# Optimization experiments

Hardware: AMD Instinct MI355X
Metric: run time of the kernel (lower is better)

The kernel has to match this reference:

```python
import jax, jax.numpy as jnp
import numpy as np
from jax import lax

D3 = 48      # manifold_dim * 3
M = 512      # mem_slots
H = 256      # slot_dim
K = 32       # topk
IN = 1024    # input_dim
ODE_HID = 128
ODE_STEPS = 2
ODE_DT = 0.5
TEMP = 1.0   # temperature buffer
LN_EPS = 1e-5


def _ln(x, g, b):
    m = jnp.mean(x, axis=-1, keepdims=True)
    v = jnp.mean(jnp.square(x - m), axis=-1, keepdims=True)
    return (x - m) * lax.rsqrt(v + LN_EPS) * g + b


def setup_inputs() -> dict:
    key = jax.random.key(0)
    ks = jax.random.split(key, 12)
    s_in = 1.0 / np.sqrt(IN)
    s_h = 1.0 / np.sqrt(H)
    s_d3 = 1.0 / np.sqrt(D3)
    s_ode = 1.0 / np.sqrt(ODE_HID)
    return {
        "x": jax.random.normal(ks[0], (16, 2048, IN), jnp.float32),
        "w1": jax.random.uniform(ks[1], (IN, D3), jnp.float32, -s_in, s_in),
        "b1": jnp.zeros((D3,), jnp.float32),
        "g1": jnp.ones((D3,), jnp.float32),
        "be1": jnp.zeros((D3,), jnp.float32),
        "wa": jax.random.uniform(ks[2], (D3, ODE_HID), jnp.float32, -s_d3, s_d3),
        "ba": jnp.zeros((ODE_HID,), jnp.float32),
        "wb": jax.random.uniform(ks[3], (ODE_HID, D3), jnp.float32, -s_ode, s_ode),
        "bb": jnp.zeros((D3,), jnp.float32),
        "mem": jax.random.normal(ks[4], (M, H), jnp.float32),
        "pos": jax.random.normal(ks[5], (M, 16, 3), jnp.float32),
        "curv": jax.random.normal(ks[6], (M, 16), jnp.float32),
        "alpha": jnp.float32(0.1),
        "wo": jax.random.uniform(ks[7], (H, IN), jnp.float32, -s_h, s_h),
        "bo": jnp.zeros((IN,), jnp.float32),
        "go": jnp.ones((IN,), jnp.float32),
        "beo": jnp.zeros((IN,), jnp.float32),
    }


def reference(x, w1, b1, g1, be1, wa, ba, wb, bb, mem, pos, curv, alpha, wo, bo, go, beo):
    # manifold projection: Linear -> LayerNorm -> GELU, viewed as (B,S,D,3)
    h = jax.nn.gelu(_ln(x @ w1 + b1, g1, be1), approximate=False)  # (B,S,48)
    # ODE evolution (2 fixed steps over the flattened manifold coords)
    for _ in range(ODE_STEPS):
        dx = jnp.tanh(h @ wa + ba) @ wb + bb
        h = h + ODE_DT * dx
    # attend: query side is detached in the original
    q = lax.stop_gradient(h)                       # (B,S,48)
    mem_pos = pos.reshape(M, -1)                   # (512,48)
    # squared pairwise L2: ||q||^2 - 2 q.m + ||m||^2
    dist = (jnp.sum(q * q, axis=-1, keepdims=True)
            - 2.0 * jnp.einsum('bsd,md->bsm', q, mem_pos)
            + jnp.sum(mem_pos * mem_pos, axis=-1))
    dist = jnp.maximum(dist, 0.0) / max(TEMP, 1e-6)
    curv_w = jnp.exp(-alpha * jnp.linalg.norm(curv, axis=-1))  # (512,)
    dist = dist * curv_w[None, None, :]
    # topk smallest distances
    neg_top, itop = lax.top_k(-dist, K)            # (B,S,K)
    w = jax.nn.softmax(neg_top, axis=-1)           # softmax(-dtop)
    slots = mem[itop]                              # (B,S,K,256) gather
    attended = jnp.einsum('bsk,bskh->bsh', w, slots)
    # output projection: Linear -> LayerNorm -> GELU
    return jax.nn.gelu(_ln(attended @ wo + bo, go, beo), approximate=False)
```

## Files before the change

### kernel.cpp

```cpp
#include <hip/hip_runtime.h>
#include <stdint.h>

typedef unsigned short u16;
typedef __attribute__((ext_vector_type(4))) short short4v;
typedef __attribute__((ext_vector_type(8))) short short8v;
typedef __attribute__((ext_vector_type(4))) float f32x4;
typedef __attribute__((address_space(1))) void gv;
typedef __attribute__((address_space(3))) void lv;

#define NTOK 32768

__device__ __forceinline__ float bf2f(u16 u){ return __uint_as_float(((uint32_t)u)<<16); }
__device__ __forceinline__ u16 f2bf(float f){
  uint32_t u = __float_as_uint(f);
  u += 0x7FFFu + ((u>>16)&1u);
  return (u16)(u>>16);
}
__device__ __forceinline__ void hilo(float v, u16& h, u16& l){
  h = f2bf(v);
  l = f2bf(v - bf2f(h));
}
__device__ __forceinline__ void tsplit(float v, u16& h, u16& l){
  uint32_t b = __float_as_uint(v);
  h = (u16)(b >> 16);
  float lf = v - __uint_as_float(b & 0xFFFF0000u);
  l = (u16)(__float_as_uint(lf) >> 16);
}
__device__ __forceinline__ void tpack8(float4 a, float4 b, short8v& hi, short8v& lo){
  float v[8] = {a.x,a.y,a.z,a.w,b.x,b.y,b.z,b.w};
  #pragma unroll
  for (int i=0;i<8;++i){ u16 h,l; tsplit(v[i],h,l); hi[i]=(short)h; lo[i]=(short)l; }
}
__device__ __forceinline__ float gelu_f(float v){ return 0.5f*v*(1.0f + erff(v*0.70710678118654752440f)); }
__device__ __forceinline__ float gelu_t(float x){
  float u = 0.7978845608028654f*(x + 0.044715f*x*x*x);
  float t = 1.0f - 2.0f/(__expf(2.0f*u) + 1.0f);
  return 0.5f*x*(1.0f + t);
}
__device__ __forceinline__ float tanh_f(float x){ return 1.0f - 2.0f/(__expf(2.0f*x)+1.0f); }

__global__ __launch_bounds__(256) void k_prep(
    const float* __restrict__ w1, const float* __restrict__ wa, const float* __restrict__ wb,
    const float* __restrict__ pos, const float* __restrict__ curv,
    const float* __restrict__ mem, const float* __restrict__ wo,
    const float* __restrict__ alpha,
    u16* __restrict__ w1s, u16* __restrict__ wah, u16* __restrict__ wbh,
    float2* __restrict__ mnw,
    u16* __restrict__ memb, u16* __restrict__ woB, u16* __restrict__ posB)
{
  int i = blockIdx.x*256 + threadIdx.x;
  if (i < 49152){ int n = i>>10, k = i&1023; u16 h,l; hilo(w1[k*48+n], h, l);
                  w1s[i] = h; w1s[49152+i] = l; return; }
  i -= 49152;
  if (i < 8192){ int u = i>>6, d = i&63; float v = (d<48) ? wa[d*128+u] : 0.f;
                 u16 h,l; hilo(v,h,l); wah[i] = h; wah[8192+i] = l; return; }
  i -= 8192;
  if (i < 6144){ int n = i>>7, u = i&127; u16 h,l; hilo(wb[u*48+n], h, l);
                 wbh[i] = h; wbh[6144+i] = l; return; }
  i -= 6144;
  if (i < 512){
    float s = 0.f;
    #pragma unroll
    for (int d=0; d<48; ++d){ float v = pos[i*48+d]; s += v*v; }
    float c2 = 0.f;
    #pragma unroll
    for (int d=0; d<16; ++d){ float v = curv[i*16+d]; c2 += v*v; }
    mnw[i] = make_float2(s, expf(-alpha[0]*sqrtf(c2)));
    return;
  }
  i -= 512;
  if (i < 131072){ memb[i] = f2bf(mem[i]); return; }
  i -= 131072;
  if (i < 262144){
    int e = i & 7, ln = (i>>3)&63, n = (i>>9)&15, cpq = (i>>13)&3, kt = i>>15;
    int col = cpq*256 + n*16 + (ln & 15);
    int k   = kt*32 + (ln >> 4)*8 + e;
    woB[i] = f2bf(wo[k*1024 + col]);
    return;
  }
  i -= 262144;
  if (i < 32768){
    int e = i & 7, ln = (i>>3)&63, n = (i>>9)&31, ks = i>>14;
    int slot = n*16 + (ln&15);
    int d = ks*32 + (ln>>4)*8 + e;
    float v = (d < 48) ? pos[slot*48 + d] : 0.f;
    u16 h,l; hilo(v,h,l);
    posB[i] = h; posB[32768+i] = l;
  }
}

__global__ __launch_bounds__(256, 2) void k_proj(
    const float* __restrict__ x, const u16* __restrict__ w1s,
    const float* __restrict__ b1, const float* __restrict__ g1, const float* __restrict__ be1,
    float* __restrict__ hout)
{
  extern __shared__ char dynp[];
  float* xsl = (float*)dynp;
  u16*   bsl = (u16*)(dynp + 49152);

  const int tid = threadIdx.x;
  const int lane = tid & 63, w = tid >> 6;
  const int l15 = lane & 15, l4 = lane >> 4;
  const int bm = blockIdx.x;
  const int arow = w*16 + l15;

  f32x4 acc[3];
  #pragma unroll
  for (int n=0; n<3; ++n) acc[n] = (f32x4){0.f,0.f,0.f,0.f};

  auto stage_x = [&](float* dst, int kt){
    #pragma unroll
    for (int j=0; j<4; ++j){
      int idx = (j*4 + w)*64 + lane;
      int row = idx >> 4, q = idx & 15;
      int chunk = q >> 1, half = q & 1;
      const float* src = x + (size_t)(bm*64 + row)*1024 + kt*64 + ((chunk ^ (row & 7))*8 + half*4);
      __builtin_amdgcn_global_load_lds((gv*)src, (lv*)(dst + (j*4 + w)*256), 16, 0, 0);
    }
  };
  auto stage_b = [&](u16* dst, int kt){
    #pragma unroll
    for (int j=0; j<3; ++j){
      int idx = (j*4 + w)*64 + lane;
      int hl = (idx >= 384) ? 1 : 0;
      int rr = idx - hl*384;
      int row = rr >> 3, ch = rr & 7;
      const u16* src = w1s + hl*49152 + (size_t)row*1024 + kt*64 + ((ch ^ (row & 7))*8);
      __builtin_amdgcn_global_load_lds((gv*)src, (lv*)(dst + (j*4 + w)*512), 16, 0, 0);
    }
  };
  auto mfma_from = [&](const float* xb, const u16* bb){
    #pragma unroll
    for (int kq=0; kq<2; ++kq){
      int chunk = kq*4 + l4;
      int phys = chunk ^ (arow & 7);
      const float* xa = xb + arow*64 + phys*8;
      float4 a0 = *(const float4*)xa;
      float4 a1 = *(const float4*)(xa + 4);
      short8v ah, al; tpack8(a0, a1, ah, al);
      #pragma unroll
      for (int n=0; n<3; ++n){
        int brow = n*16 + l15;
        int bcx = chunk ^ (brow & 7);
        short8v bh = *(const short8v*)(bb + brow*64 + bcx*8);
        short8v bl = *(const short8v*)(bb + 3072 + brow*64 + bcx*8);
        acc[n] = __builtin_amdgcn_mfma_f32_16x16x32_bf16(ah, bh, acc[n], 0, 0, 0);
        acc[n] = __builtin_amdgcn_mfma_f32_16x16x32_bf16(ah, bl, acc[n], 0, 0, 0);
        acc[n] = __builtin_amdgcn_mfma_f32_16x16x32_bf16(al, bh, acc[n], 0, 0, 0);
      }
    }
  };

  float* x0 = xsl;         float* x1 = xsl + 4096;  float* x2 = xsl + 8192;
  u16*   b0 = bsl;         u16*   b1b = bsl + 6144;

  stage_b(b0, 0);
  stage_x(x0, 0);
  stage_x(x1, 1);

  float* xc = x0; float* xn = x1; float* xn2 = x2;
  u16* bc = b0;  u16* bn = b1b;

  for (int kt = 0; kt < 15; ++kt){
    asm volatile("s_waitcnt vmcnt(4)" ::: "memory");
    __builtin_amdgcn_s_barrier();
    __builtin_amdgcn_sched_barrier(0);
    mfma_from(xc, bc);
    stage_b(bn, kt + 1);
    if (kt < 14) stage_x(xn2, kt + 2);
    { float* t = xc; xc = xn; xn = xn2; xn2 = t; }
    { u16* t = bc; bc = bn; bn = t; }
  }
  asm volatile("s_waitcnt vmcnt(0)" ::: "memory");
  __builtin_amdgcn_s_barrier();
  __builtin_amdgcn_sched_barrier(0);
  mfma_from(xc, bc);

  float b1r[3], g1r[3], e1r[3];
  #pragma unroll
  for (int n=0; n<3; ++n){ int c = n*16 + l15; b1r[n] = b1[c]; g1r[n] = g1[c]; e1r[n] = be1[c]; }
  #pragma unroll
  for (int r=0; r<4; ++r){
    float a0 = acc[0][r] + b1r[0];
    float a1 = acc[1][r] + b1r[1];
    float a2 = acc[2][r] + b1r[2];
    float s1 = a0+a1+a2;
    float s2 = a0*a0 + a1*a1 + a2*a2;
    #pragma unroll
    for (int m=1; m<16; m<<=1){ s1 += __shfl_xor(s1, m); s2 += __shfl_xor(s2, m); }
    float mean = s1 * (1.f/48.f);
    float var  = s2 * (1.f/48.f) - mean*mean;
    float rs = rsqrtf(var + 1e-5f);
    int row = bm*64 + w*16 + l4*4 + r;
    float* hb = hout + (size_t)row*48;
    hb[l15]      = gelu_f((a0-mean)*rs*g1r[0] + e1r[0]);
    hb[16+l15]   = gelu_f((a1-mean)*rs*g1r[1] + e1r[1]);
    hb[32+l15]   = gelu_f((a2-mean)*rs*g1r[2] + e1r[2]);
  }
}

__global__ __launch_bounds__(256) void k_ode(
    const float* __restrict__ hin,
    const u16* __restrict__ wah, const u16* __restrict__ wbh,
    const float* __restrict__ ba, const float* __restrict__ bb,
    float* __restrict__ hout, float* __restrict__ q2b)
{
  extern __shared__ u16 sm[];
  u16* t_hi = sm;
  u16* t_lo = sm + 16384;
  u16* h_hi = sm + 32768;
  u16* h_lo = sm + 40960;
  float* hscr = (float*)sm;

  const int tid = threadIdx.x;
  const int lane = tid & 63, w = tid >> 6;
  const int l15 = lane & 15, l4 = lane >> 4;
  const int bm = blockIdx.x;

  float4 hv4[6];
  #pragma unroll
  for (int it=0; it<6; ++it){
    int q = it*256 + tid;
    int row = q/12, c4 = q - row*12;
    hv4[it] = *(const float4*)(hin + (size_t)(bm*128 + row)*48 + c4*4);
  }
  #pragma unroll
  for (int it=0; it<6; ++it){
    int q = it*256 + tid;
    int row = q/12, c4 = q - row*12;
    *(float4*)&hscr[row*48 + c4*4] = hv4[it];
    float4 v = hv4[it];
    u16 h0,l0,h1,l1,h2,l2,h3,l3;
    tsplit(v.x,h0,l0); tsplit(v.y,h1,l1); tsplit(v.z,h2,l2); tsplit(v.w,h3,l3);
    int off = row*64 + ((c4>>1) ^ (row & 7))*8 + (c4 & 1)*4;
    short4v hv = {(short)h0,(short)h1,(short)h2,(short)h3};
    short4v lv = {(short)l0,(short)l1,(short)l2,(short)l3};
    *(short4v*)&h_hi[off] = hv;
    *(short4v*)&h_lo[off] = lv;
  }
  {
    int row = tid >> 1, ch = 6 + (tid & 1);
    int off = row*64 + (ch ^ (row & 7))*8;
    uint4 z = {0u,0u,0u,0u};
    *(uint4*)&h_hi[off] = z;
    *(uint4*)&h_lo[off] = z;
  }
  __syncthreads();

  float hreg[2][3][4];
  #pragma unroll
  for (int m=0; m<2; ++m)
    #pragma unroll
    for (int n=0; n<3; ++n)
      #pragma unroll
      for (int r=0; r<4; ++r)
        hreg[m][n][r] = hscr[(w*32 + m*16 + l4*4 + r)*48 + n*16 + l15];
  __syncthreads();

  float ba_r[8], bb_r[3];
  #pragma unroll
  for (int n=0; n<8; ++n) ba_r[n] = ba[n*16 + l15];
  #pragma unroll
  for (int n=0; n<3; ++n) bb_r[n] = bb[n*16 + l15];

  for (int s=0; s<2; ++s){
    f32x4 at[2][8];
    #pragma unroll
    for (int m=0; m<2; ++m)
      #pragma unroll
      for (int n=0; n<8; ++n) at[m][n] = (f32x4){0.f,0.f,0.f,0.f};
    #pragma unroll
    for (int kq=0; kq<2; ++kq){
      short8v ah[2], al[2];
      #pragma unroll
      for (int m=0; m<2; ++m){
        int arow = w*32 + m*16 + l15;
        int ac = (kq*4 + l4) ^ (arow & 7);
        ah[m] = *(const short8v*)&h_hi[arow*64 + ac*8];
        al[m] = *(const short8v*)&h_lo[arow*64 + ac*8];
      }
      #pragma unroll
      for (int n=0; n<8; ++n){
        const u16* bp = wah + (n*16 + l15)*64 + kq*32 + l4*8;
        short8v bh = *(const short8v*)bp;
        short8v bl = *(const short8v*)(bp + 8192);
        #pragma unroll
        for (int m=0; m<2; ++m){
          at[m][n] = __builtin_amdgcn_mfma_f32_16x16x32_bf16(ah[m], bh, at[m][n], 0, 0, 0);
          at[m][n] = __builtin_amdgcn_mfma_f32_16x16x32_bf16(ah[m], bl, at[m][n], 0, 0, 0);
          at[m][n] = __builtin_amdgcn_mfma_f32_16x16x32_bf16(al[m], bh, at[m][n], 0, 0, 0);
        }
      }
    }
    #pragma unroll
    for (int m=0; m<2; ++m)
      #pragma unroll
      for (int n=0; n<8; ++n)
        #pragma unroll
        for (int r=0; r<4; ++r){
          float tv = tanh_f(at[m][n][r] + ba_r[n]);
          u16 th, tl; tsplit(tv, th, tl);
          int row = w*32 + m*16 + l4*4 + r;
          int col = n*16 + l15;
          int c = col >> 3;
          int phys = (c & 8) | ((c & 7) ^ (row & 7));
          int off = row*128 + phys*8 + (col & 7);
          t_hi[off] = th; t_lo[off] = tl;
        }
    __syncthreads();
    f32x4 ad[2][3];
    #pragma unroll
    for (int m=0; m<2; ++m)
      #pragma unroll
      for (int n=0; n<3; ++n) ad[m][n] = (f32x4){0.f,0.f,0.f,0.f};
    #pragma unroll
    for (int kq=0; kq<4; ++kq){
      short8v ah[2], al[2];
      #pragma unroll
      for (int m=0; m<2; ++m){
        int arow = w*32 + m*16 + l15;
        int c = kq*4 + l4;
        int phys = (c & 8) | ((c & 7) ^ (arow & 7));
        ah[m] = *(const short8v*)&t_hi[arow*128 + phys*8];
        al[m] = *(const short8v*)&t_lo[arow*128 + phys*8];
      }
      #pragma unroll
      for (int n=0; n<3; ++n){
        const u16* bp = wbh + (n*16 + l15)*128 + kq*32 + l4*8;
        short8v bh = *(const short8v*)bp;
        short8v bl = *(const short8v*)(bp + 6144);
        #pragma unroll
        for (int m=0; m<2; ++m){
          ad[m][n] = __builtin_amdgcn_mfma_f32_16x16x32_bf16(ah[m], bh, ad[m][n], 0, 0, 0);
          ad[m][n] = __builtin_amdgcn_mfma_f32_16x16x32_bf16(ah[m], bl, ad[m][n], 0, 0, 0);
          ad[m][n] = __builtin_amdgcn_mfma_f32_16x16x32_bf16(al[m], bh, ad[m][n], 0, 0, 0);
        }
      }
    }
    #pragma unroll
    for (int m=0; m<2; ++m)
      #pragma unroll
      for (int n=0; n<3; ++n)
        #pragma unroll
        for (int r=0; r<4; ++r)
          hreg[m][n][r] += 0.5f*(ad[m][n][r] + bb_r[n]);
    if (s == 0){
      #pragma unroll
      for (int m=0; m<2; ++m)
        #pragma unroll
        for (int n=0; n<3; ++n)
          #pragma unroll
          for (int r=0; r<4; ++r){
            u16 hh, hl2; tsplit(hreg[m][n][r], hh, hl2);
            int row = w*32 + m*16 + l4*4 + r;
            int col = n*16 + l15;
            int off = row*64 + ((col>>3) ^ (row & 7))*8 + (col & 7);
            h_hi[off] = hh; h_lo[off] = hl2;
          }
      __syncthreads();
    }
  }
  #pragma unroll
  for (int m=0; m<2; ++m){
    #pragma unroll
    for (int r=0; r<4; ++r){
      size_t row = (size_t)(bm*128 + w*32 + m*16 + l4*4 + r);
      #pragma unroll
      for (int n=0; n<3; ++n)
        hout[row*64 + n*16 + l15] = hreg[m][n][r];
      hout[row*64 + 48 + l15] = 0.f;
      float s2 = hreg[m][0][r]*hreg[m][0][r] + hreg[m][1][r]*hreg[m][1][r] + hreg[m][2][r]*hreg[m][2][r];
      #pragma unroll
      for (int msk=1; msk<16; msk<<=1) s2 += __shfl_xor(s2, msk);
      if (l15 == 0) q2b[row] = s2;
    }
  }
}

__global__ __launch_bounds__(256, 4) void k_sel(
    const float* __restrict__ h, const float* __restrict__ q2b,
    const u16* __restrict__ posB, const float2* __restrict__ mnw,
    uint32_t* __restrict__ glist)
{
  __shared__ __align__(16) uint32_t tokKeys[2*4*528];

  const int tid = threadIdx.x;
  const int lane = tid & 63, w = tid >> 6;
  const int g = w >> 1, s = w & 1;
  const int l15 = lane & 15, l4 = lane >> 4;
  const int bm = blockIdx.x;

  const float* hrow = h + (size_t)(bm*32 + g*16 + l15)*64;
  float4 x0 = *(const float4*)(hrow + l4*8);
  float4 x1 = *(const float4*)(hrow + l4*8 + 4);
  float4 x2 = *(const float4*)(hrow + 32 + l4*8);
  float4 x3 = *(const float4*)(hrow + 32 + l4*8 + 4);
  short8v ah0, al0, ah1, al1;
  tpack8(x0, x1, ah0, al0);
  tpack8(x2, x3, ah1, al1);

  float4 q2v = *(const float4*)(q2b + bm*32 + g*16 + l4*4);
  float q2a[4] = {q2v.x, q2v.y, q2v.z, q2v.w};

  uint32_t kk[16][4];
  #pragma unroll
  for (int n=0; n<16; ++n){
    const u16* pb = posB + (size_t)(s*16 + n)*512 + lane*8;
    short8v bh0 = *(const short8v*)(pb);
    short8v bl0 = *(const short8v*)(pb + 32768);
    short8v bh1 = *(const short8v*)(pb + 16384);
    short8v bl1 = *(const short8v*)(pb + 49152);
    f32x4 acc = (f32x4){0.f,0.f,0.f,0.f};
    acc = __builtin_amdgcn_mfma_f32_16x16x32_bf16(ah0, bh0, acc, 0, 0, 0);
    acc = __builtin_amdgcn_mfma_f32_16x16x32_bf16(ah0, bl0, acc, 0, 0, 0);
    acc = __builtin_amdgcn_mfma_f32_16x16x32_bf16(al0, bh0, acc, 0, 0, 0);
    acc = __builtin_amdgcn_mfma_f32_16x16x32_bf16(ah1, bh1, acc, 0, 0, 0);
    acc = __builtin_amdgcn_mfma_f32_16x16x32_bf16(ah1, bl1, acc, 0, 0, 0);
    acc = __builtin_amdgcn_mfma_f32_16x16x32_bf16(al1, bh1, acc, 0, 0, 0);
    const int slot = s*256 + n*16 + l15;
    float2 mw = mnw[slot];
    #pragma unroll
    for (int r=0; r<4; ++r){
      float dd = fmaxf(q2a[r] + mw.x - 2.f*acc[r], 0.f) * mw.y;
      kk[n][r] = (__float_as_uint(dd) & 0xFFFFFE00u) | (uint32_t)slot;
    }
  }

  const int gbase = g*2112;
  const unsigned long long ltmask = (lane == 63) ? 0x7FFFFFFFFFFFFFFFull : ((1ull << lane) - 1ull);
  #pragma unroll
  for (int r=0; r<4; ++r){
    __syncthreads();
    #pragma unroll
    for (int n=0; n<16; ++n)
      tokKeys[gbase + l4*528 + s*256 + n*16 + l15] = kk[n][r];
    __syncthreads();
    uint32_t key8[2][8];
    #pragma unroll
    for (int j=0; j<2; ++j){
      *(uint4*)&key8[j][0] = *(const uint4*)&tokKeys[gbase + (s*2+j)*528 + lane*8];
      *(uint4*)&key8[j][4] = *(const uint4*)&tokKeys[gbase + (s*2+j)*528 + lane*8 + 4];
    }
    uint32_t p[2] = {0u,0u};
    for (int b=30; b>=0; --b){
      #pragma unroll
      for (int j=0; j<2; ++j){
        uint32_t c = p[j] | (1u<<b);
        int cnt = 0;
        #pragma unroll
        for (int i=0; i<8; ++i) cnt += (int)__popcll(__ballot(key8[j][i] < c));
        if (cnt <= 31) p[j] = c;
      }
    }
    #pragma unroll
    for (int j=0; j<2; ++j){
      size_t tok = (size_t)bm*32 + g*16 + (s*2+j)*4 + r;
      int base = 0;
      #pragma unroll
      for (int i=0; i<8; ++i){
        unsigned long long bal = __ballot(key8[j][i] <= p[j]);
        if (key8[j][i] <= p[j]){
          int idx = base + (int)__popcll(bal & ltmask);
          glist[tok*32 + idx] = key8[j][i];
        }
        base += (int)__popcll(bal);
      }
    }
  }
}

__global__ __launch_bounds__(256) void k_attend(
    const uint32_t* __restrict__ glist, const u16* __restrict__ memb,
    u16* __restrict__ att)
{
  const int lane = threadIdx.x & 63, w = threadIdx.x >> 6;
  const size_t tok = (size_t)blockIdx.x*4 + w;
  uint32_t lk[32];
  const uint4* lp = (const uint4*)(glist + tok*32);
  #pragma unroll
  for (int q=0; q<8; ++q) *(uint4*)&lk[q*4] = lp[q];
  uint32_t km = lk[0];
  #pragma unroll
  for (int i=1; i<32; ++i) km = min(km, lk[i]);
  const float dminf = __uint_as_float(km & 0xFFFFFE00u);

  float den = 0.f, a0=0.f, a1=0.f, a2=0.f, a3=0.f;
  #pragma unroll
  for (int i=0; i<32; ++i){
    float dk = __uint_as_float(lk[i] & 0xFFFFFE00u);
    int slot = (int)(lk[i] & 511u);
    float wg = __expf(dminf - dk);
    den += wg;
    uint2 mv = ((const uint2*)(memb + (size_t)slot*256))[lane];
    a0 += wg*bf2f((u16)(mv.x & 0xFFFFu));
    a1 += wg*bf2f((u16)(mv.x >> 16));
    a2 += wg*bf2f((u16)(mv.y & 0xFFFFu));
    a3 += wg*bf2f((u16)(mv.y >> 16));
  }
  float inv = 1.f/den;
  uint32_t o0 = (uint32_t)f2bf(a0*inv) | ((uint32_t)f2bf(a1*inv) << 16);
  uint32_t o1 = (uint32_t)f2bf(a2*inv) | ((uint32_t)f2bf(a3*inv) << 16);
  ((uint2*)(att + tok*256))[lane] = make_uint2(o0, o1);
}

__global__ __launch_bounds__(1024, 4) void k_out(
    const u16* __restrict__ A, const u16* __restrict__ woB, const float* __restrict__ bo,
    const float* __restrict__ go, const float* __restrict__ beo, float* __restrict__ out)
{
  __shared__ u16 Asl[64*256];
  __shared__ float red[64*4*2];

  const int tid = threadIdx.x;
  const int lane = tid & 63, w = tid >> 6;
  const int tg = w >> 2, cp = w & 3;
  const int l15 = lane & 15, l4 = lane >> 4;
  const int bm = blockIdx.x;

  #pragma unroll
  for (int j=0; j<2; ++j){
    int idx = j*1024 + tid;
    int row = idx >> 5, ch = idx & 31;
    int gc = (ch & 24) | ((ch & 7) ^ (row & 7));
    uint4 v = *(const uint4*)(A + (size_t)(bm*64 + row)*256 + gc*8);
    *(uint4*)&Asl[row*256 + ch*8] = v;
  }
  __syncthreads();

  f32x4 acc[16];
  #pragma unroll
  for (int n=0; n<16; ++n) acc[n] = (f32x4){0.f,0.f,0.f,0.f};

  const int arow = tg*16 + l15;
  #pragma unroll
  for (int kt=0; kt<8; ++kt){
    int c = kt*4 + l4;
    int aphys = (c & 24) | ((c & 7) ^ (arow & 7));
    short8v af = *(const short8v*)&Asl[arow*256 + aphys*8];
    const u16* bbase = woB + ((size_t)(kt*4 + cp)*16)*512 + lane*8;
    #pragma unroll
    for (int n=0; n<16; ++n){
      short8v bf = *(const short8v*)(bbase + n*512);
      acc[n] = __builtin_amdgcn_mfma_f32_16x16x32_bf16(af, bf, acc[n], 0, 0, 0);
    }
  }

  float bor[16];
  #pragma unroll
  for (int n=0; n<16; ++n) bor[n] = bo[cp*256 + n*16 + l15];
  float s1[4] = {0.f,0.f,0.f,0.f}, s2[4] = {0.f,0.f,0.f,0.f};
  #pragma unroll
  for (int n=0; n<16; ++n)
    #pragma unroll
    for (int r=0; r<4; ++r){
      float v = acc[n][r] + bor[n];
      acc[n][r] = v;
      s1[r] += v; s2[r] += v*v;
    }
  #pragma unroll
  for (int r=0; r<4; ++r){
    #pragma unroll
    for (int m=1; m<16; m<<=1){ s1[r] += __shfl_xor(s1[r], m); s2[r] += __shfl_xor(s2[r], m); }
  }
  if (l15 == 0){
    #pragma unroll
    for (int r=0; r<4; ++r){
      int t = tg*16 + l4*4 + r;
      red[(t*4 + cp)*2 + 0] = s1[r];
      red[(t*4 + cp)*2 + 1] = s2[r];
    }
  }
  __syncthreads();
  float mean[4], rs[4];
  #pragma unroll
  for (int r=0; r<4; ++r){
    int t = tg*16 + l4*4 + r;
    float a1 = red[(t*4+0)*2] + red[(t*4+1)*2] + red[(t*4+2)*2] + red[(t*4+3)*2];
    float a2 = red[(t*4+0)*2+1] + red[(t*4+1)*2+1] + red[(t*4+2)*2+1] + red[(t*4+3)*2+1];
    mean[r] = a1 * (1.f/1024.f);
    float var = a2 * (1.f/1024.f) - mean[r]*mean[r];
    rs[r] = rsqrtf(var + 1e-5f);
  }
  #pragma unroll
  for (int n=0; n<16; ++n){
    int col = cp*256 + n*16 + l15;
    float g = go[col], e = beo[col];
    #pragma unroll
    for (int r=0; r<4; ++r){
      size_t row = (size_t)bm*64 + tg*16 + l4*4 + r;
      out[row*1024 + col] = gelu_t((acc[n][r] - mean[r])*rs[r]*g + e);
    }
  }
}

extern "C" void kernel_launch(void* const* d_in, const int* in_sizes, int n_in,
                              void* d_out, int out_size, void* d_ws, size_t ws_size,
                              hipStream_t stream) {
  const float* x    = (const float*)d_in[0];
  const float* w1   = (const float*)d_in[1];
  const float* b1   = (const float*)d_in[2];
  const float* g1   = (const float*)d_in[3];
  const float* be1  = (const float*)d_in[4];
  const float* wa   = (const float*)d_in[5];
  const float* ba   = (const float*)d_in[6];
  const float* wb   = (const float*)d_in[7];
  const float* bb   = (const float*)d_in[8];
  const float* mem  = (const float*)d_in[9];
  const float* pos  = (const float*)d_in[10];
  const float* curv = (const float*)d_in[11];
  const float* alpha= (const float*)d_in[12];
  const float* wo   = (const float*)d_in[13];
  const float* bo   = (const float*)d_in[14];
  const float* go   = (const float*)d_in[15];
  const float* beo  = (const float*)d_in[16];
  float* out = (float*)d_out;

  char* ws = (char*)d_ws;
  size_t o = 0;
  auto take = [&](size_t b) -> char* { char* p = ws + o; o += (b + 255) & ~(size_t)255; return p; };
  char*  regA   = take(67108864);
  float* hbuf48 = (float*)regA;
  float* hbuf64 = (float*)(regA + 6291456);
  float* q2b    = (float*)(regA + 6291456 + 8388608);
  u16*   att    = (u16*)take(16777216);
  u16*   w1s    = (u16*)take(196608);
  u16*   wah    = (u16*)take(32768);
  u16*   wbh    = (u16*)take(24576);
  float2* mnw   = (float2*)take(4096);
  u16*   memb   = (u16*)take(262144);
  u16*   woB    = (u16*)take(524288);
  u16*   posB   = (u16*)take(131072);
  uint32_t* glist = (uint32_t*)take(4194304);

  hipFuncSetAttribute((const void*)k_ode, hipFuncAttributeMaxDynamicSharedMemorySize, 98304);
  hipFuncSetAttribute((const void*)k_proj, hipFuncAttributeMaxDynamicSharedMemorySize, 73728);

  k_prep<<<1914, 256, 0, stream>>>(w1, wa, wb, pos, curv, mem, wo, alpha,
                                   w1s, wah, wbh, mnw, memb, woB, posB);
  k_proj<<<512, 256, 73728, stream>>>(x, w1s, b1, g1, be1, hbuf48);
  k_ode<<<256, 256, 98304, stream>>>(hbuf48, wah, wbh, ba, bb, hbuf64, q2b);
  k_sel<<<1024, 256, 0, stream>>>(hbuf64, q2b, posB, mnw, glist);
  k_attend<<<8192, 256, 0, stream>>>(glist, memb, att);
  k_out<<<512, 1024, 0, stream>>>(att, woB, bo, go, beo, out);
  (void)in_sizes; (void)n_in; (void)out_size; (void)ws_size;
}
```

Measured before the change: 254.1 us.

## Retile output GEMM so each wave covers all 64 rows by 64 columns

The output projection kernel changes its warp tiling. Previously each of the 16 waves computed 16 rows by 256 columns and streamed 16 B fragments from global memory per k-step. Now each wave computes all 64 rows by 64 columns, reading 4 A fragments from LDS and 4 B fragments from global memory and reusing them across a 4x4 MFMA tile. This cuts global weight traffic per block. In exchange the LayerNorm reduction now spans all 16 waves, so it uses two padded LDS arrays and an extra shuffle reduction.

```diff
diff --git a/kernel.cpp b/kernel.cpp
--- a/kernel.cpp
+++ b/kernel.cpp
@@ -508,11 +508,11 @@
     const float* __restrict__ go, const float* __restrict__ beo, float* __restrict__ out)
 {
   __shared__ u16 Asl[64*256];
-  __shared__ float red[64*4*2];
+  __shared__ float red1[16*65];
+  __shared__ float red2[16*65];
 
   const int tid = threadIdx.x;
   const int lane = tid & 63, w = tid >> 6;
-  const int tg = w >> 2, cp = w & 3;
   const int l15 = lane & 15, l4 = lane >> 4;
   const int bm = blockIdx.x;
 
@@ -526,69 +526,103 @@
   }
   __syncthreads();
 
-  f32x4 acc[16];
-  #pragma unroll
-  for (int n=0; n<16; ++n) acc[n] = (f32x4){0.f,0.f,0.f,0.f};
-
-  const int arow = tg*16 + l15;
+  f32x4 acc[4][4];
+  #pragma unroll
+  for (int m=0; m<4; ++m)
+    #pragma unroll
+    for (int n=0; n<4; ++n) acc[m][n] = (f32x4){0.f,0.f,0.f,0.f};
+
   #pragma unroll
   for (int kt=0; kt<8; ++kt){
-    int c = kt*4 + l4;
-    int aphys = (c & 24) | ((c & 7) ^ (arow & 7));
-    short8v af = *(const short8v*)&Asl[arow*256 + aphys*8];
-    const u16* bbase = woB + ((size_t)(kt*4 + cp)*16)*512 + lane*8;
-    #pragma unroll
-    for (int n=0; n<16; ++n){
+    const int c = kt*4 + l4;
+    short8v af[4];
+    #pragma unroll
+    for (int m=0; m<4; ++m){
+      int arow = m*16 + l15;
+      int aphys = (c & 24) | ((c & 7) ^ (arow & 7));
+      af[m] = *(const short8v*)&Asl[arow*256 + aphys*8];
+    }
+    const u16* bbase = woB + ((size_t)kt*64 + w*4)*512 + lane*8;
+    #pragma unroll
+    for (int n=0; n<4; ++n){
       short8v bf = *(const short8v*)(bbase + n*512);
-      acc[n] = __builtin_amdgcn_mfma_f32_16x16x32_bf16(af, bf, acc[n], 0, 0, 0);
-    }
-  }
-
-  float bor[16];
-  #pragma unroll
-  for (int n=0; n<16; ++n) bor[n] = bo[cp*256 + n*16 + l15];
-  float s1[4] = {0.f,0.f,0.f,0.f}, s2[4] = {0.f,0.f,0.f,0.f};
-  #pragma unroll
-  for (int n=0; n<16; ++n)
+      #pragma unroll
+      for (int m=0; m<4; ++m)
+        acc[m][n] = __builtin_amdgcn_mfma_f32_16x16x32_bf16(af[m], bf, acc[m][n], 0, 0, 0);
+    }
+  }
+
+  float bor[4];
+  #pragma unroll
+  for (int n=0; n<4; ++n) bor[n] = bo[w*64 + n*16 + l15];
+
+  float s1[4][4], s2[4][4];
+  #pragma unroll
+  for (int m=0; m<4; ++m)
+    #pragma unroll
+    for (int r=0; r<4; ++r){ s1[m][r] = 0.f; s2[m][r] = 0.f; }
+  #pragma unroll
+  for (int m=0; m<4; ++m)
+    #pragma unroll
+    for (int n=0; n<4; ++n)
+      #pragma unroll
+      for (int r=0; r<4; ++r){
+        float v = acc[m][n][r] + bor[n];
+        acc[m][n][r] = v;
+        s1[m][r] += v; s2[m][r] += v*v;
+      }
+  #pragma unroll
+  for (int m=0; m<4; ++m)
     #pragma unroll
     for (int r=0; r<4; ++r){
-      float v = acc[n][r] + bor[n];
-      acc[n][r] = v;
-      s1[r] += v; s2[r] += v*v;
-    }
-  #pragma unroll
-  for (int r=0; r<4; ++r){
-    #pragma unroll
-    for (int m=1; m<16; m<<=1){ s1[r] += __shfl_xor(s1[r], m); s2[r] += __shfl_xor(s2[r], m); }
-  }
+      #pragma unroll
+      for (int msk=1; msk<16; msk<<=1){
+        s1[m][r] += __shfl_xor(s1[m][r], msk);
+        s2[m][r] += __shfl_xor(s2[m][r], msk);
+      }
+    }
   if (l15 == 0){
     #pragma unroll
+    for (int m=0; m<4; ++m)
+      #pragma unroll
+      for (int r=0; r<4; ++r){
+        int t = m*16 + l4*4 + r;
+        red1[w*65 + t] = s1[m][r];
+        red2[w*65 + t] = s2[m][r];
+      }
+  }
+  __syncthreads();
+
+  float mean[4][4], rs[4][4];
+  #pragma unroll
+  for (int m=0; m<4; ++m)
+    #pragma unroll
     for (int r=0; r<4; ++r){
-      int t = tg*16 + l4*4 + r;
-      red[(t*4 + cp)*2 + 0] = s1[r];
-      red[(t*4 + cp)*2 + 1] = s2[r];
-    }
-  }
-  __syncthreads();
-  float mean[4], rs[4];
-  #pragma unroll
-  for (int r=0; r<4; ++r){
-    int t = tg*16 + l4*4 + r;
-    float a1 = red[(t*4+0)*2] + red[(t*4+1)*2] + red[(t*4+2)*2] + red[(t*4+3)*2];
-    float a2 = red[(t*4+0)*2+1] + red[(t*4+1)*2+1] + red[(t*4+2)*2+1] + red[(t*4+3)*2+1];
-    mean[r] = a1 * (1.f/1024.f);
-    float var = a2 * (1.f/1024.f) - mean[r]*mean[r];
-    rs[r] = rsqrtf(var + 1e-5f);
-  }
-  #pragma unroll
-  for (int n=0; n<16; ++n){
-    int col = cp*256 + n*16 + l15;
+      int t = m*16 + l4*4 + r;
+      float a1 = red1[l15*65 + t];
+      float a2 = red2[l15*65 + t];
+      #pragma unroll
+      for (int msk=1; msk<16; msk<<=1){
+        a1 += __shfl_xor(a1, msk);
+        a2 += __shfl_xor(a2, msk);
+      }
+      float mu = a1 * (1.f/1024.f);
+      float var = a2 * (1.f/1024.f) - mu*mu;
+      mean[m][r] = mu;
+      rs[m][r] = rsqrtf(var + 1e-5f);
+    }
+
+  #pragma unroll
+  for (int n=0; n<4; ++n){
+    int col = w*64 + n*16 + l15;
     float g = go[col], e = beo[col];
     #pragma unroll
-    for (int r=0; r<4; ++r){
-      size_t row = (size_t)bm*64 + tg*16 + l4*4 + r;
-      out[row*1024 + col] = gelu_t((acc[n][r] - mean[r])*rs[r]*g + e);
-    }
+    for (int m=0; m<4; ++m)
+      #pragma unroll
+      for (int r=0; r<4; ++r){
+        size_t row = (size_t)bm*64 + m*16 + l4*4 + r;
+        out[row*1024 + col] = gelu_t((acc[m][n][r] - mean[m][r])*rs[m][r]*g + e);
+      }
   }
 }
 
```

Result: slower. 266.6 us (+4.9%).
